# Kernel optimization log

Hardware: AMD Instinct MI355X
Metric: run time of the kernel (lower is better)

Reference implementation:

```python
import jax, jax.numpy as jnp
import numpy as np

EMBED = 1024
DFF = 4096


def _layernorm(x, g, b, eps=1e-5):
    mu = jnp.mean(x, axis=-1, keepdims=True)
    var = jnp.var(x, axis=-1, keepdims=True)
    return (x - mu) * jax.lax.rsqrt(var + eps) * g + b


def setup_inputs() -> dict:
    key = jax.random.key(0)
    ks = jax.random.split(key, 14)
    s = 1.0 / np.sqrt(EMBED)
    sf = 1.0 / np.sqrt(DFF)
    d = {
        "src": jax.random.normal(ks[0], (4, 2048, EMBED), dtype=jnp.float32),
        "Wq": jax.random.uniform(ks[1], (EMBED, EMBED), jnp.float32, -s, s),
        "bq": jnp.zeros((EMBED,), jnp.float32),
        "Wk": jax.random.uniform(ks[2], (EMBED, EMBED), jnp.float32, -s, s),
        "bk": jnp.zeros((EMBED,), jnp.float32),
        "Wv": jax.random.uniform(ks[3], (EMBED, EMBED), jnp.float32, -s, s),
        "bv": jnp.zeros((EMBED,), jnp.float32),
        "Wo": jax.random.uniform(ks[4], (EMBED, EMBED), jnp.float32, -s, s),
        "bo": jnp.zeros((EMBED,), jnp.float32),
        "W1": jax.random.uniform(ks[5], (EMBED, DFF), jnp.float32, -s, s),
        "b1": jnp.zeros((DFF,), jnp.float32),
        "W2": jax.random.uniform(ks[6], (DFF, EMBED), jnp.float32, -sf, sf),
        "b2": jnp.zeros((EMBED,), jnp.float32),
        "g1": jnp.ones((EMBED,), jnp.float32),
        "be1": jnp.zeros((EMBED,), jnp.float32),
        "g2": jnp.ones((EMBED,), jnp.float32),
        "be2": jnp.zeros((EMBED,), jnp.float32),
    }
    return d


def reference(src, Wq, bq, Wk, bk, Wv, bv, Wo, bo, W1, b1, W2, b2, g1, be1, g2, be2):
    # Q/K/V projections: [b, s, d]
    Q = src @ Wq + bq
    K = src @ Wk + bk
    V = src @ Wv + bv
    # Single-head, UNSCALED attention (faithful to source: no 1/sqrt(d), num_heads unused)
    scores = jnp.einsum("bqd,bkd->bqk", Q, K)  # [b, s, s]
    weights = jax.nn.softmax(scores, axis=-1)
    attn = jnp.einsum("bqk,bkd->bqd", weights, V)
    attn = attn @ Wo + bo
    x = _layernorm(src + attn, g1, be1)
    ff = jax.nn.relu(x @ W1 + b1) @ W2 + b2
    return _layernorm(x + ff, g2, be2)
```

## Files before the change

kernel.cpp:

```cpp
#include <hip/hip_runtime.h>
#include <stdint.h>

typedef unsigned short u16;
typedef _Float16 v8h __attribute__((ext_vector_type(8)));
typedef float v4f __attribute__((ext_vector_type(4)));

static __device__ __forceinline__ float h2f(u16 u) {
    union { u16 s; _Float16 h; } v; v.s = u; return (float)v.h;
}
static __device__ __forceinline__ u16 f2h(float f) {
    union { u16 s; _Float16 h; } v; v.h = (_Float16)f; return v.s;
}

static __device__ __forceinline__ void gload_lds16(const u16* g, const u16* l) {
    __builtin_amdgcn_global_load_lds(
        (const __attribute__((address_space(1))) uint32_t*)(uintptr_t)g,
        (__attribute__((address_space(3))) uint32_t*)(uintptr_t)l,
        16, 0, 0);
}

__global__ __launch_bounds__(256) void cvt_f16(const float* __restrict__ in,
                                               u16* __restrict__ out, int n8) {
    const int i = blockIdx.x * 256 + threadIdx.x;
    if (i >= n8) return;
    const float4 a = ((const float4*)in)[2 * i];
    const float4 b = ((const float4*)in)[2 * i + 1];
    u16 o[8] = {f2h(a.x), f2h(a.y), f2h(a.z), f2h(a.w),
                f2h(b.x), f2h(b.y), f2h(b.z), f2h(b.w)};
    *(uint4*)(out + (size_t)i * 8) = *(const uint4*)o;
}

__global__ __launch_bounds__(256) void transpose_all(
    const float* __restrict__ Wq, const float* __restrict__ Wk,
    const float* __restrict__ Wv, const float* __restrict__ Wo,
    const float* __restrict__ W1, const float* __restrict__ W2,
    u16* __restrict__ WqkvT, u16* __restrict__ WoT,
    u16* __restrict__ W1T, u16* __restrict__ W2T)
{
    int t = blockIdx.x;
    const float* in; u16* out; long ldi, ldo; int xt;
    if (t < 1024)      {            in = Wq; out = WqkvT;               ldi = 1024; ldo = 1024; xt = 32; }
    else if (t < 2048) { t -= 1024; in = Wk; out = WqkvT + 1024*1024;   ldi = 1024; ldo = 1024; xt = 32; }
    else if (t < 3072) { t -= 2048; in = Wv; out = WqkvT + 2*1024*1024; ldi = 1024; ldo = 1024; xt = 32; }
    else if (t < 4096) { t -= 3072; in = Wo; out = WoT;                 ldi = 1024; ldo = 1024; xt = 32; }
    else if (t < 8192) { t -= 4096; in = W1; out = W1T;                 ldi = 4096; ldo = 1024; xt = 128; }
    else               { t -= 8192; in = W2; out = W2T;                 ldi = 1024; ldo = 4096; xt = 32; }
    const int c0 = (t % xt) * 32, r0 = (t / xt) * 32;
    __shared__ float tile[32][33];
    for (int i = threadIdx.y; i < 32; i += 8)
        tile[i][threadIdx.x] = in[(long)(r0 + i) * ldi + c0 + threadIdx.x];
    __syncthreads();
    for (int i = threadIdx.y; i < 32; i += 8)
        out[(long)(c0 + i) * ldo + r0 + threadIdx.x] = f2h(tile[threadIdx.x][i]);
}

template<int OMODE, int BIAS, bool RELU, int NX, int NY, int NZ>
__global__ __launch_bounds__(512, 4) void gemm256n(
    const u16* __restrict__ A, long lda, long Asb,
    const u16* __restrict__ B, long ldb, long Bsb,
    void* __restrict__ Cv, long ldc, long Csb, u16* __restrict__ C1,
    const float* __restrict__ bias, const float* __restrict__ bias2,
    const float* __restrict__ bias3, int K)
{
    constexpr int NWG = NX * NY * NZ;
    static_assert(NWG % 8 == 0, "XCD swizzle needs nwg % 8 == 0");
    alignas(16) __shared__ u16 As[4 * 8192];
    alignas(16) __shared__ u16 Bs[2 * 4096];

    const int tid = threadIdx.x;
    const int lane = tid & 63, wave = tid >> 6;
    const int l16 = lane & 15, quad = lane >> 4;
    const int wm = wave >> 1;
    const int wn = wave & 1;

    const int lin = blockIdx.x;
    const int tl = (lin & 7) * (NWG / 8) + (lin >> 3);
    const int xe = tl % NX;
    const int ye = (tl / NX) % NY;
    const int zb = tl / (NX * NY);
    const long m0 = (long)ye * 256;
    const long n0 = (long)xe * 128;

    const u16* Aop = A + (long)zb * Asb;
    const u16* Bop = B + (long)zb * Bsb;

    const int srow = tid >> 2;
    const int sq = (tid & 3) ^ ((tid >> 3) & 3);
    const long gaofs0 = (m0 + srow) * lda + sq * 8;
    const long gaofs1 = gaofs0 + 128 * lda;
    const long gbofs0 = (n0 + srow) * ldb + sq * 8;
    const int wv512n = wave * 512;

    const int swzE = (quad ^ ((l16 >> 1) & 3)) * 8;
    const int aRow = (wm * 64 + l16) * 32 + swzE;
    const int bRow = (wn * 64 + l16) * 32 + swzE;

    v4f acc[4][4];
#pragma unroll
    for (int i = 0; i < 4; ++i)
#pragma unroll
        for (int j = 0; j < 4; ++j)
            acc[i][j] = (v4f){0.f, 0.f, 0.f, 0.f};
    v8h bf[4];

#define STAGE_A(RIDX, KP) do { \
        u16* lb_ = As + (RIDX) * 8192 + wv512n; \
        gload_lds16(Aop + gaofs0 + (KP), lb_); \
        gload_lds16(Aop + gaofs1 + (KP), lb_ + 4096); } while (0)
#define STAGE_B(SLOT, KP) do { \
        gload_lds16(Bop + gbofs0 + (KP), Bs + (SLOT) * 4096 + wv512n); } while (0)

#define PHASE(BUF, KH, CH, EVENW, STG) { \
        if (EVENW) asm volatile("s_waitcnt vmcnt(2)" ::: "memory"); \
        const u16* Ar_ = As + ((BUF) * 2 + (KH)) * 8192 + aRow + (CH) * 1024; \
        v8h af0 = *(const v8h*)(Ar_); \
        v8h af1 = *(const v8h*)(Ar_ + 512); \
        if ((CH) == 0) { \
            const u16* Br_ = Bs + (KH) * 4096 + bRow; \
            bf[0] = *(const v8h*)(Br_); \
            bf[1] = *(const v8h*)(Br_ + 512); \
            bf[2] = *(const v8h*)(Br_ + 1024); \
            bf[3] = *(const v8h*)(Br_ + 1536); \
        } \
        STG; \
        __builtin_amdgcn_s_barrier(); \
        asm volatile("s_waitcnt lgkmcnt(0)" ::: "memory"); \
        __builtin_amdgcn_s_setprio(1); \
        acc[(CH)*2+0][0] = __builtin_amdgcn_mfma_f32_16x16x32_f16(af0, bf[0], acc[(CH)*2+0][0], 0, 0, 0); \
        acc[(CH)*2+0][1] = __builtin_amdgcn_mfma_f32_16x16x32_f16(af0, bf[1], acc[(CH)*2+0][1], 0, 0, 0); \
        acc[(CH)*2+0][2] = __builtin_amdgcn_mfma_f32_16x16x32_f16(af0, bf[2], acc[(CH)*2+0][2], 0, 0, 0); \
        acc[(CH)*2+0][3] = __builtin_amdgcn_mfma_f32_16x16x32_f16(af0, bf[3], acc[(CH)*2+0][3], 0, 0, 0); \
        acc[(CH)*2+1][0] = __builtin_amdgcn_mfma_f32_16x16x32_f16(af1, bf[0], acc[(CH)*2+1][0], 0, 0, 0); \
        acc[(CH)*2+1][1] = __builtin_amdgcn_mfma_f32_16x16x32_f16(af1, bf[1], acc[(CH)*2+1][1], 0, 0, 0); \
        acc[(CH)*2+1][2] = __builtin_amdgcn_mfma_f32_16x16x32_f16(af1, bf[2], acc[(CH)*2+1][2], 0, 0, 0); \
        acc[(CH)*2+1][3] = __builtin_amdgcn_mfma_f32_16x16x32_f16(af1, bf[3], acc[(CH)*2+1][3], 0, 0, 0); \
        __builtin_amdgcn_s_setprio(0); \
        __builtin_amdgcn_s_barrier(); \
    }

    STAGE_A(0, 0);  STAGE_B(0, 0);
    STAGE_A(1, 32); STAGE_B(1, 32);
    STAGE_A(2, 64);
    asm volatile("s_waitcnt vmcnt(5)" ::: "memory");
    __builtin_amdgcn_s_barrier();

    const int NT = K >> 7;
#pragma unroll 1
    for (int t = 0; t < NT; ++t) {
        const long kb = (long)t * 128;
        long kp2  = kb + 128; if (kp2  >= K) kp2  = 0;
        long kp2b = kb + 160; if (kp2b >= K) kp2b = 0;
        long kp3  = kb + 192; if (kp3  >= K) kp3  = 0;

        PHASE(0, 0, 0, false, STAGE_A(3, kb + 96))
        PHASE(0, 0, 1, true,  STAGE_B(0, kb + 64))
        PHASE(0, 1, 0, false, STAGE_A(0, kp2))
        PHASE(0, 1, 1, true,  STAGE_B(1, kb + 96))
        PHASE(1, 0, 0, false, STAGE_A(1, kp2b))
        PHASE(1, 0, 1, true,  STAGE_B(0, kp2))
        PHASE(1, 1, 0, false, STAGE_A(2, kp3))
        PHASE(1, 1, 1, true,  STAGE_B(1, kp2b))
    }

    asm volatile("s_waitcnt vmcnt(0) lgkmcnt(0)" ::: "memory");
    __builtin_amdgcn_s_barrier();

#undef PHASE
#undef STAGE_A
#undef STAGE_B

    float bv[4];
#pragma unroll
    for (int j = 0; j < 4; ++j) {
        const long col = n0 + wn * 64 + j * 16 + l16;
        if (BIAS == 0) bv[j] = 0.f;
        else if (BIAS == 1) bv[j] = bias[col];
        else {
            const int sel = (int)(col >> 10);
            const float* bp = sel == 0 ? bias : (sel == 1 ? bias2 : bias3);
            bv[j] = bp[col & 1023];
        }
    }

    if (OMODE == 3 && n0 >= 2048) {
        const long bb = m0 >> 11, mb = m0 & 2047;
        u16* C = C1 + bb * Csb;
#pragma unroll
        for (int j = 0; j < 4; ++j) {
            const long col = n0 - 2048 + wn * 64 + j * 16 + l16;
            u16* pc = C + col * 2048 + mb + wm * 64 + quad * 4;
#pragma unroll
            for (int i = 0; i < 4; ++i) {
                u16 o[4];
#pragma unroll
                for (int r = 0; r < 4; ++r) {
                    float val = acc[i][j][r] + bv[j];
                    if (RELU) val = fmaxf(val, 0.f);
                    o[r] = f2h(val);
                }
                *(uint2*)(pc + i * 16) = *(const uint2*)o;
            }
        }
    } else {
        const long cb = (OMODE == 3 ? 0 : (long)zb * Csb)
                      + (m0 + wm * 64 + quad * 4) * ldc + (n0 + wn * 64 + l16);
        u16* p0 = (u16*)Cv + cb;
#pragma unroll
        for (int i = 0; i < 4; ++i)
#pragma unroll
            for (int r = 0; r < 4; ++r) {
                u16* prow = p0 + (long)(i * 16 + r) * ldc;
#pragma unroll
                for (int j = 0; j < 4; ++j) {
                    float val = acc[i][j][r] + bv[j];
                    if (RELU) val = fmaxf(val, 0.f);
                    prow[j * 16] = f2h(val);
                }
            }
    }
}

__global__ __launch_bounds__(256) void softmax_rows(u16* __restrict__ S) {
    const long row = blockIdx.x;
    u16* p = S + row * 2048;
    const int t = threadIdx.x;
    float v[8];
    float mx = -1e30f;
#pragma unroll
    for (int i = 0; i < 8; ++i) { v[i] = h2f(p[t + i * 256]); mx = fmaxf(mx, v[i]); }
    __shared__ float red[256];
    red[t] = mx; __syncthreads();
    for (int off = 128; off > 0; off >>= 1) {
        if (t < off) red[t] = fmaxf(red[t], red[t + off]);
        __syncthreads();
    }
    mx = red[0]; __syncthreads();
    float sum = 0.f;
#pragma unroll
    for (int i = 0; i < 8; ++i) { v[i] = __expf(v[i] - mx); sum += v[i]; }
    red[t] = sum; __syncthreads();
    for (int off = 128; off > 0; off >>= 1) {
        if (t < off) red[t] += red[t + off];
        __syncthreads();
    }
    const float inv = 1.f / red[0];
#pragma unroll
    for (int i = 0; i < 8; ++i) p[t + i * 256] = f2h(v[i] * inv);
}

__global__ __launch_bounds__(256) void ln_one(
    const float* __restrict__ a, const u16* __restrict__ bb,
    const float* __restrict__ g, const float* __restrict__ be,
    u16* __restrict__ out16)
{
    const long base = (long)blockIdx.x * 1024;
    const int t = threadIdx.x;
    float v[4]; float s = 0.f, ss = 0.f;
#pragma unroll
    for (int i = 0; i < 4; ++i) {
        const int c = t + i * 256;
        const float x = a[base + c] + h2f(bb[base + c]);
        v[i] = x; s += x; ss += x * x;
    }
    __shared__ float rs[256], rss[256];
    rs[t] = s; rss[t] = ss; __syncthreads();
    for (int off = 128; off > 0; off >>= 1) {
        if (t < off) { rs[t] += rs[t + off]; rss[t] += rss[t + off]; }
        __syncthreads();
    }
    const float mean = rs[0] * (1.f / 1024.f);
    const float var = rss[0] * (1.f / 1024.f) - mean * mean;
    const float rstd = rsqrtf(var + 1e-5f);
#pragma unroll
    for (int i = 0; i < 4; ++i) {
        const int c = t + i * 256;
        out16[base + c] = f2h((v[i] - mean) * rstd * g[c] + be[c]);
    }
}

__global__ __launch_bounds__(256) void ln_two(
    const u16* __restrict__ a, const u16* __restrict__ bb,
    const float* __restrict__ g, const float* __restrict__ be,
    float* __restrict__ out)
{
    const long base = (long)blockIdx.x * 1024;
    const int t = threadIdx.x;
    float v[4]; float s = 0.f, ss = 0.f;
#pragma unroll
    for (int i = 0; i < 4; ++i) {
        const int c = t + i * 256;
        const float x = h2f(a[base + c]) + h2f(bb[base + c]);
        v[i] = x; s += x; ss += x * x;
    }
    __shared__ float rs[256], rss[256];
    rs[t] = s; rss[t] = ss; __syncthreads();
    for (int off = 128; off > 0; off >>= 1) {
        if (t < off) { rs[t] += rs[t + off]; rss[t] += rss[t + off]; }
        __syncthreads();
    }
    const float mean = rs[0] * (1.f / 1024.f);
    const float var = rss[0] * (1.f / 1024.f) - mean * mean;
    const float rstd = rsqrtf(var + 1e-5f);
#pragma unroll
    for (int i = 0; i < 4; ++i) {
        const int c = t + i * 256;
        out[base + c] = (v[i] - mean) * rstd * g[c] + be[c];
    }
}

extern "C" void kernel_launch(void* const* d_in, const int* in_sizes, int n_in,
                              void* d_out, int out_size, void* d_ws, size_t ws_size,
                              hipStream_t stream) {
    (void)in_sizes; (void)n_in; (void)out_size; (void)ws_size;
    constexpr long S = 2048, E = 1024, F = 4096, M = 8192;

    const float* src = (const float*)d_in[0];
    const float* Wq  = (const float*)d_in[1];
    const float* bq  = (const float*)d_in[2];
    const float* Wk  = (const float*)d_in[3];
    const float* bk  = (const float*)d_in[4];
    const float* Wv  = (const float*)d_in[5];
    const float* bv  = (const float*)d_in[6];
    const float* Wo  = (const float*)d_in[7];
    const float* bo  = (const float*)d_in[8];
    const float* W1  = (const float*)d_in[9];
    const float* b1  = (const float*)d_in[10];
    const float* W2  = (const float*)d_in[11];
    const float* b2  = (const float*)d_in[12];
    const float* g1  = (const float*)d_in[13];
    const float* be1 = (const float*)d_in[14];
    const float* g2  = (const float*)d_in[15];
    const float* be2 = (const float*)d_in[16];

    char* ws = (char*)d_ws;
    size_t off = 0;
    auto take = [&](size_t bytes) {
        char* p = ws + off;
        off += (bytes + 255) & ~(size_t)255;
        return p;
    };
    const size_t MB16 = 16777216;
    u16*   srcH  = (u16*)take(MB16);
    u16*   WqkvT = (u16*)take(3 * E * E * 2);
    u16*   WoT   = (u16*)take(E * E * 2);
    u16*   W1T   = (u16*)take(F * E * 2);
    u16*   W2T   = (u16*)take(E * F * 2);
    char*  B0    = take(2 * MB16);
    char*  B1    = take(MB16);
    char*  B2    = take(4ull * S * S * 4);
    char*  B3    = take(MB16);
    char*  B4    = take(MB16);

    u16*   QK    = (u16*)B0;
    u16*   VT    = (u16*)B1;
    u16*   Sh    = (u16*)B2;
    u16*   hf    = (u16*)B2;
    u16*   attn  = (u16*)B3;
    u16*   xh    = (u16*)B3;
    u16*   attnO = (u16*)B4;
    u16*   ffO   = (u16*)B4;

    dim3 blk(256), blk5(512), tb(32, 8);

    cvt_f16<<<dim3(M * E / 8 / 256), blk, 0, stream>>>(src, srcH, M * E / 8);

    transpose_all<<<dim3(12288), tb, 0, stream>>>(Wq, Wk, Wv, Wo, W1, W2,
                                                  WqkvT, WoT, W1T, W2T);

    gemm256n<3, 3, false, 24, 32, 1><<<dim3(24 * 32), blk5, 0, stream>>>(
        srcH, E, 0, WqkvT, E, 0, QK, 2 * E, E * S, VT, bq, bk, bv, E);

    gemm256n<0, 0, false, 16, 8, 4><<<dim3(16 * 8 * 4), blk5, 0, stream>>>(
        QK, 2 * E, S * 2 * E, QK + E, 2 * E, S * 2 * E,
        Sh, S, S * S, nullptr, nullptr, nullptr, nullptr, E);

    softmax_rows<<<dim3(M), blk, 0, stream>>>(Sh);

    gemm256n<0, 0, false, 8, 8, 4><<<dim3(8 * 8 * 4), blk5, 0, stream>>>(
        Sh, S, S * S, VT, S, E * S,
        attn, E, S * E, nullptr, nullptr, nullptr, nullptr, S);

    gemm256n<0, 1, false, 8, 32, 1><<<dim3(8 * 32), blk5, 0, stream>>>(
        attn, E, 0, WoT, E, 0, attnO, E, 0, nullptr, bo, nullptr, nullptr, E);

    ln_one<<<dim3(M), blk, 0, stream>>>(src, attnO, g1, be1, xh);

    gemm256n<0, 1, true, 32, 32, 1><<<dim3(32 * 32), blk5, 0, stream>>>(
        xh, E, 0, W1T, E, 0, hf, F, 0, nullptr, b1, nullptr, nullptr, E);

    gemm256n<0, 1, false, 8, 32, 1><<<dim3(8 * 32), blk5, 0, stream>>>(
        hf, F, 0, W2T, F, 0, ffO, E, 0, nullptr, b2, nullptr, nullptr, F);

    ln_two<<<dim3(M), blk, 0, stream>>>(xh, ffO, g2, be2, (float*)d_out);
}
```

Before: 496.2 us.

## Add 256x128-tile 32x32x16 MFMA GEMM kernel for FFN up-projection

Adds a new GEMM kernel using 32x32x16 f16 MFMA instructions with 256x128 output tiles, a multi-buffered global-to-LDS pipeline, XCD-aware block swizzling and priority boosting around MFMA bursts. It replaces the previous gemm256n launch for the W1 projection with ReLU. The aim is better MFMA throughput and overlap of loads with compute for this largest GEMM. The tile shape changes (n tile 128, NX=32 covers 4096 columns) and the deep LDS buffering may limit occupancy or add scheduling risk.

```diff
diff --git a/kernel.cpp b/kernel.cpp
--- a/kernel.cpp
+++ b/kernel.cpp
@@ -4,6 +4,7 @@
 typedef unsigned short u16;
 typedef _Float16 v8h __attribute__((ext_vector_type(8)));
 typedef float v4f __attribute__((ext_vector_type(4)));
+typedef float v16f __attribute__((ext_vector_type(16)));
 
 static __device__ __forceinline__ float h2f(u16 u) {
     union { u16 s; _Float16 h; } v; v.s = u; return (float)v.h;
@@ -220,6 +221,138 @@
     }
 }
 
+template<int BIAS, bool RELU, int NX, int NY, int NZ>
+__global__ __launch_bounds__(512, 4) void gemm32(
+    const u16* __restrict__ A, long lda,
+    const u16* __restrict__ B, long ldb,
+    u16* __restrict__ C, long ldc,
+    const float* __restrict__ bias, int K)
+{
+    constexpr int NWG = NX * NY * NZ;
+    static_assert(NWG % 8 == 0, "XCD swizzle needs nwg % 8 == 0");
+    alignas(16) __shared__ u16 As[4 * 8192];
+    alignas(16) __shared__ u16 Bs[2 * 4096];
+
+    const int tid = threadIdx.x;
+    const int lane = tid & 63, wave = tid >> 6;
+    const int l32 = lane & 31, koct = lane >> 5;
+    const int wm = wave >> 1;
+    const int wn = wave & 1;
+
+    const int lin = blockIdx.x;
+    const int tl = (lin & 7) * (NWG / 8) + (lin >> 3);
+    const int xe = tl % NX;
+    const int ye = (tl / NX) % NY;
+    const long m0 = (long)ye * 256;
+    const long n0 = (long)xe * 128;
+
+    const int srow = tid >> 2;
+    const int sq = (tid & 3) ^ ((tid >> 3) & 3);
+    const long gaofs0 = (m0 + srow) * lda + sq * 8;
+    const long gaofs1 = gaofs0 + 128 * lda;
+    const long gbofs0 = (n0 + srow) * ldb + sq * 8;
+    const int wv512n = wave * 512;
+
+    const int amask = (l32 >> 1) & 3;
+    const int s0 = (koct ^ amask) * 8;
+    const int s1 = ((2 + koct) ^ amask) * 8;
+    const int aBase = (wm * 64 + l32) * 32;
+    const int bBase = (wn * 64 + l32) * 32;
+
+    v16f acc[2][2];
+#pragma unroll
+    for (int i = 0; i < 2; ++i)
+#pragma unroll
+        for (int j = 0; j < 2; ++j)
+#pragma unroll
+            for (int r = 0; r < 16; ++r) acc[i][j][r] = 0.f;
+    v8h bf00, bf01, bf10, bf11;
+
+#define STAGE_A(RIDX, KP) do { \
+        u16* lb_ = As + (RIDX) * 8192 + wv512n; \
+        gload_lds16(A + gaofs0 + (KP), lb_); \
+        gload_lds16(A + gaofs1 + (KP), lb_ + 4096); } while (0)
+#define STAGE_B(SLOT, KP) do { \
+        gload_lds16(B + gbofs0 + (KP), Bs + (SLOT) * 4096 + wv512n); } while (0)
+
+#define PHASE(BUF, KH, CH, EVENW, STG) { \
+        if (EVENW) asm volatile("s_waitcnt vmcnt(2)" ::: "memory"); \
+        const u16* Ar_ = As + ((BUF) * 2 + (KH)) * 8192 + aBase + (CH) * 1024; \
+        v8h af0 = *(const v8h*)(Ar_ + s0); \
+        v8h af1 = *(const v8h*)(Ar_ + s1); \
+        if ((CH) == 0) { \
+            const u16* Br_ = Bs + (KH) * 4096 + bBase; \
+            bf00 = *(const v8h*)(Br_ + s0); \
+            bf01 = *(const v8h*)(Br_ + s1); \
+            bf10 = *(const v8h*)(Br_ + 1024 + s0); \
+            bf11 = *(const v8h*)(Br_ + 1024 + s1); \
+        } \
+        STG; \
+        __builtin_amdgcn_s_barrier(); \
+        asm volatile("s_waitcnt lgkmcnt(0)" ::: "memory"); \
+        __builtin_amdgcn_s_setprio(1); \
+        acc[CH][0] = __builtin_amdgcn_mfma_f32_32x32x16_f16(af0, bf00, acc[CH][0], 0, 0, 0); \
+        acc[CH][1] = __builtin_amdgcn_mfma_f32_32x32x16_f16(af0, bf10, acc[CH][1], 0, 0, 0); \
+        acc[CH][0] = __builtin_amdgcn_mfma_f32_32x32x16_f16(af1, bf01, acc[CH][0], 0, 0, 0); \
+        acc[CH][1] = __builtin_amdgcn_mfma_f32_32x32x16_f16(af1, bf11, acc[CH][1], 0, 0, 0); \
+        __builtin_amdgcn_s_setprio(0); \
+        __builtin_amdgcn_s_barrier(); \
+    }
+
+    STAGE_A(0, 0);  STAGE_B(0, 0);
+    STAGE_A(1, 32); STAGE_B(1, 32);
+    STAGE_A(2, 64);
+    asm volatile("s_waitcnt vmcnt(5)" ::: "memory");
+    __builtin_amdgcn_s_barrier();
+
+    const int NT = K >> 7;
+#pragma unroll 1
+    for (int t = 0; t < NT; ++t) {
+        const long kb = (long)t * 128;
+        long kp2  = kb + 128; if (kp2  >= K) kp2  = 0;
+        long kp2b = kb + 160; if (kp2b >= K) kp2b = 0;
+        long kp3  = kb + 192; if (kp3  >= K) kp3  = 0;
+
+        PHASE(0, 0, 0, false, STAGE_A(3, kb + 96))
+        PHASE(0, 0, 1, true,  STAGE_B(0, kb + 64))
+        PHASE(0, 1, 0, false, STAGE_A(0, kp2))
+        PHASE(0, 1, 1, true,  STAGE_B(1, kb + 96))
+        PHASE(1, 0, 0, false, STAGE_A(1, kp2b))
+        PHASE(1, 0, 1, true,  STAGE_B(0, kp2))
+        PHASE(1, 1, 0, false, STAGE_A(2, kp3))
+        PHASE(1, 1, 1, true,  STAGE_B(1, kp2b))
+    }
+
+    asm volatile("s_waitcnt vmcnt(0) lgkmcnt(0)" ::: "memory");
+    __builtin_amdgcn_s_barrier();
+
+#undef PHASE
+#undef STAGE_A
+#undef STAGE_B
+
+    float bv[2];
+#pragma unroll
+    for (int j = 0; j < 2; ++j) {
+        const long col = n0 + wn * 64 + j * 32 + l32;
+        bv[j] = (BIAS == 1) ? bias[col] : 0.f;
+    }
+
+#pragma unroll
+    for (int rb = 0; rb < 2; ++rb)
+#pragma unroll
+        for (int cb = 0; cb < 2; ++cb) {
+            const long col = n0 + wn * 64 + cb * 32 + l32;
+            u16* pc = C + (m0 + wm * 64 + rb * 32 + 4 * koct) * ldc + col;
+#pragma unroll
+            for (int reg = 0; reg < 16; ++reg) {
+                const long row = (reg & 3) + 8 * (reg >> 2);
+                float val = acc[rb][cb][reg] + bv[cb];
+                if (RELU) val = fmaxf(val, 0.f);
+                pc[row * ldc] = f2h(val);
+            }
+        }
+}
+
 __global__ __launch_bounds__(256) void softmax_rows(u16* __restrict__ S) {
     const long row = blockIdx.x;
     u16* p = S + row * 2048;
@@ -385,8 +518,8 @@
 
     ln_one<<<dim3(M), blk, 0, stream>>>(src, attnO, g1, be1, xh);
 
-    gemm256n<0, 1, true, 32, 32, 1><<<dim3(32 * 32), blk5, 0, stream>>>(
-        xh, E, 0, W1T, E, 0, hf, F, 0, nullptr, b1, nullptr, nullptr, E);
+    gemm32<1, true, 32, 32, 1><<<dim3(32 * 32), blk5, 0, stream>>>(
+        xh, E, W1T, E, hf, F, b1, E);
 
     gemm256n<0, 1, false, 8, 32, 1><<<dim3(8 * 32), blk5, 0, stream>>>(
         hf, F, 0, W2T, F, 0, ffO, E, 0, nullptr, b2, nullptr, nullptr, F);
```

Result: slower. 514.5 us (+3.7%).
